# Kernel optimization log

Measured on AMD Instinct MI355X. Metric: run time of the kernel, lower is better.

The kernel has to match this reference:

```python
import jax, jax.numpy as jnp
import numpy as np

DECAY = 0.99
EPS = 1e-05
COMMIT = 0.25


def setup_inputs() -> dict:
    key = jax.random.key(0)
    k1, k2 = jax.random.split(key)
    dim, n_embed = 256, 8192
    z = jax.random.normal(k1, (32, 32, 32, dim), dtype=jnp.float32)
    embed = jax.random.normal(k2, (dim, n_embed), dtype=jnp.float32)
    cluster_size = jnp.zeros((n_embed,), dtype=jnp.float32)
    embed_avg = embed  # torch init: embed_avg = embed.clone()
    return {"z": z, "embed": embed, "cluster_size": cluster_size, "embed_avg": embed_avg}


def reference(z, embed, cluster_size, embed_avg):
    dim, n_embed = embed.shape
    flatten = z.reshape(-1, dim)                       # [N, D]
    # squared L2 distance to each code: ||f||^2 - 2 f.E + ||E||^2
    dist = ((flatten ** 2).sum(1, keepdims=True)
            - 2.0 * flatten @ embed
            + (embed ** 2).sum(0, keepdims=True))      # [N, K]
    ind = jnp.argmin(dist, axis=1)                     # [N]
    quantize = jnp.take(embed.T, ind, axis=0).reshape(z.shape)
    embed_ind = ind.reshape(z.shape[:-1])

    # EMA codebook update (training mode), via segment_sum instead of a dense one-hot
    counts = jax.ops.segment_sum(jnp.ones_like(ind, dtype=flatten.dtype), ind,
                                 num_segments=n_embed)          # [K]
    embed_sum = jax.ops.segment_sum(flatten, ind,
                                    num_segments=n_embed).T     # [D, K]
    cluster_size_new = cluster_size * DECAY + (1.0 - DECAY) * counts
    embed_avg_new = embed_avg * DECAY + (1.0 - DECAY) * embed_sum
    n = cluster_size_new.sum()
    cs = (cluster_size_new + EPS) / (n + n_embed * EPS) * n
    embed_new = embed_avg_new / cs[None, :]

    diff = COMMIT * jnp.mean((jax.lax.stop_gradient(quantize) - z) ** 2)
    quantize_st = z + jax.lax.stop_gradient(quantize - z)  # straight-through
    return quantize_st, diff, embed_ind, embed_new
```

## Files before the change

kernel.cpp:

```cpp
#include <hip/hip_runtime.h>
#include <hip/hip_bf16.h>

#define D 256
#define K 8192
#define NTOT 32768
#define BM 128
#define BN2 128
#define BD 32
#define CSPLIT 4
#define CT_PER (K / CSPLIT / BN2)

typedef __bf16 bf16x8 __attribute__((ext_vector_type(8)));
typedef float f32x4 __attribute__((ext_vector_type(4)));

__device__ __forceinline__ void gl_lds16(const void* g, void* l) {
    __builtin_amdgcn_global_load_lds(
        (__attribute__((address_space(1))) void*)(g),
        (__attribute__((address_space(3))) void*)(l), 16, 0, 0);
}

__device__ __forceinline__ unsigned int enc_f32(float f) {
    unsigned int u = __float_as_uint(f);
    return (u & 0x80000000u) ? ~u : (u | 0x80000000u);
}

__device__ __forceinline__ unsigned short f2bfu(float x) {
    __hip_bfloat16 h = __float2bfloat16(x);
    return __builtin_bit_cast(unsigned short, h);
}
__device__ __forceinline__ float bfu2f(unsigned short u) {
    return __bfloat162float(__builtin_bit_cast(__hip_bfloat16, u));
}

__global__ __launch_bounds__(256)
void conv_F(const float* __restrict__ z, unsigned short* __restrict__ Fhi,
            unsigned short* __restrict__ Flo) {
    int i4 = blockIdx.x * 256 + threadIdx.x;
    float4 v = ((const float4*)z)[i4];
    ushort4 h, l;
    h.x = f2bfu(v.x); l.x = f2bfu(v.x - bfu2f(h.x));
    h.y = f2bfu(v.y); l.y = f2bfu(v.y - bfu2f(h.y));
    h.z = f2bfu(v.z); l.z = f2bfu(v.z - bfu2f(h.z));
    h.w = f2bfu(v.w); l.w = f2bfu(v.w - bfu2f(h.w));
    ((ushort4*)Fhi)[i4] = h;
    ((ushort4*)Flo)[i4] = l;
}

__global__ __launch_bounds__(256)
void conv_E(const float* __restrict__ E, unsigned short* __restrict__ EhiT,
            unsigned short* __restrict__ EloT, float* __restrict__ ET,
            float* __restrict__ enorm) {
    __shared__ float tile[64][65];
    int tid = threadIdx.x;
    int k0 = blockIdx.x * 64, d0 = blockIdx.y * 64;
#pragma unroll
    for (int it = 0; it < 16; ++it) {
        int idx = it * 256 + tid;
        int dr = idx >> 6, kc = idx & 63;
        tile[kc][dr] = E[(d0 + dr) * K + k0 + kc];
    }
    __syncthreads();
#pragma unroll
    for (int it = 0; it < 16; ++it) {
        int idx = it * 256 + tid;
        int kr = idx >> 6, dc = idx & 63;
        float v = tile[kr][dc];
        unsigned short h = f2bfu(v);
        int o = (k0 + kr) * D + d0 + dc;
        EhiT[o] = h;
        EloT[o] = f2bfu(v - bfu2f(h));
        ET[o] = v;
        float p = v * v;
#pragma unroll
        for (int off = 32; off; off >>= 1) p += __shfl_down(p, off);
        if ((tid & 63) == 0) atomicAdd(&enorm[k0 + kr], p);
    }
}

__global__ __launch_bounds__(256)
void mfma_dist_argmin(const unsigned short* __restrict__ Fhi,
                      const unsigned short* __restrict__ Flo,
                      const unsigned short* __restrict__ EhiT,
                      const unsigned short* __restrict__ EloT,
                      const float* __restrict__ enorm,
                      unsigned long long* __restrict__ bestpack) {
    __shared__ unsigned short Ah[BM * BD], Al[BM * BD], Bh[BN2 * BD], Bl[BN2 * BD];

    const int tid = threadIdx.x;
    const int wave = tid >> 6;
    const int lane = tid & 63;
    const int qd = lane >> 4;
    const int ln = lane & 15;
    const int wm = (wave >> 1) * 64;
    const int wn = (wave & 1) * 64;
    const int n0 = blockIdx.x * BM;
    const int c0 = blockIdx.y * (K / CSPLIT);
    const int r_ = tid >> 2;
    const int s_sw = (tid & 3) ^ ((tid >> 3) & 3);
    const int csw = (qd ^ ((ln >> 1) & 3)) * 8;

    int aro[4], bro[4];
#pragma unroll
    for (int mi = 0; mi < 4; ++mi) aro[mi] = (wm + mi * 16 + ln) * BD + csw;
#pragma unroll
    for (int ni = 0; ni < 4; ++ni) bro[ni] = (wn + ni * 16 + ln) * BD + csw;

    float bestv[16];
    int besti[16];
#pragma unroll
    for (int i = 0; i < 16; ++i) { bestv[i] = 3.402823466e38f; besti[i] = 0; }

    for (int ct = 0; ct < CT_PER; ++ct) {
        const int cb = c0 + ct * BN2;
        f32x4 acc[4][4];
#pragma unroll
        for (int mi = 0; mi < 4; ++mi)
#pragma unroll
            for (int ni = 0; ni < 4; ++ni) acc[mi][ni] = (f32x4){0.f, 0.f, 0.f, 0.f};

        for (int d0 = 0; d0 < D; d0 += BD) {
            __syncthreads();
#pragma unroll
            for (int it = 0; it < 2; ++it) {
                const int ga = (n0 + it * 64 + r_) * D + d0 + s_sw * 8;
                const int gb = (cb + it * 64 + r_) * D + d0 + s_sw * 8;
                const int lo = it * 2048 + wave * 512;
                gl_lds16(Fhi + ga, &Ah[lo]);
                gl_lds16(Flo + ga, &Al[lo]);
                gl_lds16(EhiT + gb, &Bh[lo]);
                gl_lds16(EloT + gb, &Bl[lo]);
            }
            __syncthreads();

            bf16x8 a0[4], b0[4], b1[4];
#pragma unroll
            for (int mi = 0; mi < 4; ++mi) a0[mi] = *(const bf16x8*)&Ah[aro[mi]];
#pragma unroll
            for (int ni = 0; ni < 4; ++ni) b0[ni] = *(const bf16x8*)&Bh[bro[ni]];
#pragma unroll
            for (int mi = 0; mi < 4; ++mi)
#pragma unroll
                for (int ni = 0; ni < 4; ++ni)
                    acc[mi][ni] = __builtin_amdgcn_mfma_f32_16x16x32_bf16(
                        a0[mi], b0[ni], acc[mi][ni], 0, 0, 0);
#pragma unroll
            for (int ni = 0; ni < 4; ++ni) b1[ni] = *(const bf16x8*)&Bl[bro[ni]];
#pragma unroll
            for (int mi = 0; mi < 4; ++mi)
#pragma unroll
                for (int ni = 0; ni < 4; ++ni)
                    acc[mi][ni] = __builtin_amdgcn_mfma_f32_16x16x32_bf16(
                        a0[mi], b1[ni], acc[mi][ni], 0, 0, 0);
#pragma unroll
            for (int mi = 0; mi < 4; ++mi) a0[mi] = *(const bf16x8*)&Al[aro[mi]];
#pragma unroll
            for (int mi = 0; mi < 4; ++mi)
#pragma unroll
                for (int ni = 0; ni < 4; ++ni)
                    acc[mi][ni] = __builtin_amdgcn_mfma_f32_16x16x32_bf16(
                        a0[mi], b0[ni], acc[mi][ni], 0, 0, 0);
        }

#pragma unroll
        for (int ni = 0; ni < 4; ++ni) {
            int k = cb + wn + ni * 16 + ln;
            float en = enorm[k];
#pragma unroll
            for (int mi = 0; mi < 4; ++mi) {
                f32x4 a = acc[mi][ni];
#pragma unroll
                for (int r = 0; r < 4; ++r) {
                    float dist = en - 2.0f * a[r];
                    int bi = mi * 4 + r;
                    if (dist < bestv[bi]) { bestv[bi] = dist; besti[bi] = k; }
                }
            }
        }
    }

#pragma unroll
    for (int mi = 0; mi < 4; ++mi) {
#pragma unroll
        for (int r = 0; r < 4; ++r) {
            int bi = mi * 4 + r;
            float v = bestv[bi];
            int ix = besti[bi];
#pragma unroll
            for (int off = 1; off < 16; off <<= 1) {
                float v2 = __shfl_xor(v, off);
                int i2 = __shfl_xor(ix, off);
                if (v2 < v || (v2 == v && i2 < ix)) { v = v2; ix = i2; }
            }
            if (ln == 0) {
                int m = n0 + wm + mi * 16 + qd * 4 + r;
                unsigned long long pack =
                    ((unsigned long long)enc_f32(v) << 32) | (unsigned int)ix;
                atomicMin(&bestpack[m], pack);
            }
        }
    }
}

#define ROWS_PER_BLOCK 16
__global__ __launch_bounds__(256)
void assign_apply(const float* __restrict__ z,
                  const float* __restrict__ ET,
                  const unsigned long long* __restrict__ bestpack,
                  float* __restrict__ out_q, float* __restrict__ out_ind,
                  float* __restrict__ out_diff,
                  float* __restrict__ counts, float* __restrict__ esumT) {
    const int tx = threadIdx.x;
    const int rbase = blockIdx.x * ROWS_PER_BLOCK;
    float part = 0.f;
#pragma unroll 4
    for (int r = 0; r < ROWS_PER_BLOCK; ++r) {
        int n = rbase + r;
        unsigned long long p = bestpack[n];
        int idx = (int)(p & 0xFFFFFFFFull);
        float f = z[n * D + tx];
        float q = ET[idx * D + tx];
        out_q[n * D + tx] = q;
        float dd = q - f;
        part += dd * dd;
        atomicAdd(&esumT[idx * D + tx], f);
        if (tx == 0) {
            atomicAdd(&counts[idx], 1.0f);
            out_ind[n] = (float)idx;
        }
    }
#pragma unroll
    for (int off = 32; off; off >>= 1) part += __shfl_down(part, off);
    __shared__ float wsum[4];
    if ((tx & 63) == 0) wsum[tx >> 6] = part;
    __syncthreads();
    if (tx == 0) {
        float t = wsum[0] + wsum[1] + wsum[2] + wsum[3];
        atomicAdd(out_diff, t * (0.25f / 8388608.0f));
    }
}

__global__ __launch_bounds__(1024)
void csn_sum(const float* __restrict__ cs_in, const float* __restrict__ counts,
             float* __restrict__ csn, float* __restrict__ nsum) {
    const float decay = 0.99f;
    const float omd = 0.01f;
    int k = blockIdx.x * 1024 + threadIdx.x;
    float v = decay * cs_in[k] + omd * counts[k];
    csn[k] = v;
    float p = v;
#pragma unroll
    for (int off = 32; off; off >>= 1) p += __shfl_down(p, off);
    __shared__ float red[16];
    if ((threadIdx.x & 63) == 0) red[threadIdx.x >> 6] = p;
    __syncthreads();
    if (threadIdx.x == 0) {
        float t = 0.f;
#pragma unroll
        for (int i = 0; i < 16; ++i) t += red[i];
        atomicAdd(nsum, t);
    }
}

__global__ __launch_bounds__(256)
void finalize(const float* __restrict__ eavg, const float* __restrict__ esumT,
              const float* __restrict__ csn, const float* __restrict__ nsum,
              float* __restrict__ out_enew) {
    const float decay = 0.99f;
    const float omd = 0.01f;
    const float keps = (float)(8192 * 1e-5);
    int idx = blockIdx.x * 256 + threadIdx.x;
    float nv = nsum[0];
    int k = idx & (K - 1);
    int d = idx >> 13;
    float avg_new = decay * eavg[idx] + omd * esumT[k * D + d];
    float cs = (csn[k] + 1e-5f) / (nv + keps) * nv;
    out_enew[idx] = avg_new / cs;
}

extern "C" void kernel_launch(void* const* d_in, const int* in_sizes, int n_in,
                              void* d_out, int out_size, void* d_ws, size_t ws_size,
                              hipStream_t stream) {
    const float* z = (const float*)d_in[0];
    const float* embed = (const float*)d_in[1];
    const float* cs_in = (const float*)d_in[2];
    const float* eavg = (const float*)d_in[3];

    float* out = (float*)d_out;
    float* out_q = out;
    float* out_diff = out + 8388608;
    float* out_ind = out + 8388609;
    float* out_enew = out + 8421377;

    char* ws = (char*)d_ws;
    unsigned long long* bestpack = (unsigned long long*)ws;
    float* enorm = (float*)(ws + 262144);
    float* counts = (float*)(ws + 294912);
    float* csn = (float*)(ws + 327680);
    float* nsum = (float*)(ws + 360448);
    float* esumT = (float*)(ws + 360704);
    unsigned short* Fhi = (unsigned short*)(ws + 8749312);
    unsigned short* Flo = (unsigned short*)(ws + 25526528);
    unsigned short* EhiT = (unsigned short*)(ws + 42303744);
    unsigned short* EloT = (unsigned short*)(ws + 46498048);
    float* ET = (float*)(ws + 50692352);

    hipMemsetAsync(bestpack, 0xFF, NTOT * 8, stream);
    hipMemsetAsync(ws + 262144, 0, 8749312 - 262144, stream);
    hipMemsetAsync(out_diff, 0, 4, stream);

    conv_F<<<NTOT * D / 4 / 256, 256, 0, stream>>>(z, Fhi, Flo);
    conv_E<<<dim3(K / 64, D / 64), 256, 0, stream>>>(embed, EhiT, EloT, ET, enorm);
    mfma_dist_argmin<<<dim3(NTOT / BM, CSPLIT), 256, 0, stream>>>(Fhi, Flo, EhiT, EloT,
                                                                  enorm, bestpack);
    assign_apply<<<NTOT / ROWS_PER_BLOCK, 256, 0, stream>>>(z, ET, bestpack, out_q,
                                                            out_ind, out_diff, counts, esumT);
    csn_sum<<<K / 1024, 1024, 0, stream>>>(cs_in, counts, csn, nsum);
    finalize<<<(D * K) / 256, 256, 0, stream>>>(eavg, esumT, csn, nsum, out_enew);
}
```

Baseline: 600.0 us.

## Fuse conversion kernels, halve codebook split, vectorize assign and finalize, merge memsets

Merges the z and codebook bf16 split conversions into one launch, and halves the codebook split of the distance/argmin kernel so there are fewer blocks but each does more work. It hoists the code-norm loads ahead of the MFMA loop. The argmin packing switches to an inverted key with atomicMax so the workspace can be cleared with a single zero memset. The assign and finalize kernels are vectorized to float4 per lane, cutting launch and memory overhead at the cost of changed occupancy and access patterns.

After: 781.7 us. 30.3% more time.

```diff
diff --git a/kernel.cpp b/kernel.cpp
--- a/kernel.cpp
+++ b/kernel.cpp
@@ -7,7 +7,7 @@
 #define BM 128
 #define BN2 128
 #define BD 32
-#define CSPLIT 4
+#define CSPLIT 2
 #define CT_PER (K / CSPLIT / BN2)
 
 typedef __bf16 bf16x8 __attribute__((ext_vector_type(8)));
@@ -32,27 +32,29 @@
     return __bfloat162float(__builtin_bit_cast(__hip_bfloat16, u));
 }
 
+#define CONVF_BLOCKS (NTOT * D / 4 / 256)
 __global__ __launch_bounds__(256)
-void conv_F(const float* __restrict__ z, unsigned short* __restrict__ Fhi,
-            unsigned short* __restrict__ Flo) {
-    int i4 = blockIdx.x * 256 + threadIdx.x;
-    float4 v = ((const float4*)z)[i4];
-    ushort4 h, l;
-    h.x = f2bfu(v.x); l.x = f2bfu(v.x - bfu2f(h.x));
-    h.y = f2bfu(v.y); l.y = f2bfu(v.y - bfu2f(h.y));
-    h.z = f2bfu(v.z); l.z = f2bfu(v.z - bfu2f(h.z));
-    h.w = f2bfu(v.w); l.w = f2bfu(v.w - bfu2f(h.w));
-    ((ushort4*)Fhi)[i4] = h;
-    ((ushort4*)Flo)[i4] = l;
-}
-
-__global__ __launch_bounds__(256)
-void conv_E(const float* __restrict__ E, unsigned short* __restrict__ EhiT,
-            unsigned short* __restrict__ EloT, float* __restrict__ ET,
-            float* __restrict__ enorm) {
+void conv_all(const float* __restrict__ z, unsigned short* __restrict__ Fhi,
+              unsigned short* __restrict__ Flo, const float* __restrict__ E,
+              unsigned short* __restrict__ EhiT, unsigned short* __restrict__ EloT,
+              float* __restrict__ ET, float* __restrict__ enorm) {
+    int bx = blockIdx.x;
+    int tid = threadIdx.x;
+    if (bx < CONVF_BLOCKS) {
+        int i4 = bx * 256 + tid;
+        float4 v = ((const float4*)z)[i4];
+        ushort4 h, l;
+        h.x = f2bfu(v.x); l.x = f2bfu(v.x - bfu2f(h.x));
+        h.y = f2bfu(v.y); l.y = f2bfu(v.y - bfu2f(h.y));
+        h.z = f2bfu(v.z); l.z = f2bfu(v.z - bfu2f(h.z));
+        h.w = f2bfu(v.w); l.w = f2bfu(v.w - bfu2f(h.w));
+        ((ushort4*)Fhi)[i4] = h;
+        ((ushort4*)Flo)[i4] = l;
+        return;
+    }
     __shared__ float tile[64][65];
-    int tid = threadIdx.x;
-    int k0 = blockIdx.x * 64, d0 = blockIdx.y * 64;
+    int idx2 = bx - CONVF_BLOCKS;
+    int k0 = (idx2 & 127) * 64, d0 = (idx2 >> 7) * 64;
 #pragma unroll
     for (int it = 0; it < 16; ++it) {
         int idx = it * 256 + tid;
@@ -112,6 +114,10 @@
 
     for (int ct = 0; ct < CT_PER; ++ct) {
         const int cb = c0 + ct * BN2;
+        float en[4];
+#pragma unroll
+        for (int ni = 0; ni < 4; ++ni) en[ni] = enorm[cb + wn + ni * 16 + ln];
+
         f32x4 acc[4][4];
 #pragma unroll
         for (int mi = 0; mi < 4; ++mi)
@@ -164,13 +170,12 @@
 #pragma unroll
         for (int ni = 0; ni < 4; ++ni) {
             int k = cb + wn + ni * 16 + ln;
-            float en = enorm[k];
 #pragma unroll
             for (int mi = 0; mi < 4; ++mi) {
                 f32x4 a = acc[mi][ni];
 #pragma unroll
                 for (int r = 0; r < 4; ++r) {
-                    float dist = en - 2.0f * a[r];
+                    float dist = en[ni] - 2.0f * a[r];
                     int bi = mi * 4 + r;
                     if (dist < bestv[bi]) { bestv[bi] = dist; besti[bi] = k; }
                 }
@@ -193,15 +198,15 @@
             }
             if (ln == 0) {
                 int m = n0 + wm + mi * 16 + qd * 4 + r;
-                unsigned long long pack =
-                    ((unsigned long long)enc_f32(v) << 32) | (unsigned int)ix;
-                atomicMin(&bestpack[m], pack);
+                unsigned long long key =
+                    ((unsigned long long)(~enc_f32(v)) << 32) | (unsigned)(8191 - ix);
+                atomicMax(&bestpack[m], key);
             }
         }
     }
 }
 
-#define ROWS_PER_BLOCK 16
+#define AA_ROWS 32
 __global__ __launch_bounds__(256)
 void assign_apply(const float* __restrict__ z,
                   const float* __restrict__ ET,
@@ -209,21 +214,26 @@
                   float* __restrict__ out_q, float* __restrict__ out_ind,
                   float* __restrict__ out_diff,
                   float* __restrict__ counts, float* __restrict__ esumT) {
-    const int tx = threadIdx.x;
-    const int rbase = blockIdx.x * ROWS_PER_BLOCK;
+    const int wave = threadIdx.x >> 6;
+    const int lane = threadIdx.x & 63;
+    const int rbase = blockIdx.x * AA_ROWS + wave * (AA_ROWS / 4);
     float part = 0.f;
-#pragma unroll 4
-    for (int r = 0; r < ROWS_PER_BLOCK; ++r) {
+#pragma unroll
+    for (int r = 0; r < AA_ROWS / 4; ++r) {
         int n = rbase + r;
         unsigned long long p = bestpack[n];
-        int idx = (int)(p & 0xFFFFFFFFull);
-        float f = z[n * D + tx];
-        float q = ET[idx * D + tx];
-        out_q[n * D + tx] = q;
-        float dd = q - f;
-        part += dd * dd;
-        atomicAdd(&esumT[idx * D + tx], f);
-        if (tx == 0) {
+        int idx = 8191 - (int)(p & 0xFFFFFFFFull);
+        float4 f = ((const float4*)z)[n * 64 + lane];
+        float4 q = ((const float4*)ET)[idx * 64 + lane];
+        ((float4*)out_q)[n * 64 + lane] = q;
+        float dx = q.x - f.x, dy = q.y - f.y, dz = q.z - f.z, dw = q.w - f.w;
+        part += dx * dx + dy * dy + dz * dz + dw * dw;
+        float* eb = esumT + idx * D + lane * 4;
+        atomicAdd(eb + 0, f.x);
+        atomicAdd(eb + 1, f.y);
+        atomicAdd(eb + 2, f.z);
+        atomicAdd(eb + 3, f.w);
+        if (lane == 0) {
             atomicAdd(&counts[idx], 1.0f);
             out_ind[n] = (float)idx;
         }
@@ -231,9 +241,9 @@
 #pragma unroll
     for (int off = 32; off; off >>= 1) part += __shfl_down(part, off);
     __shared__ float wsum[4];
-    if ((tx & 63) == 0) wsum[tx >> 6] = part;
+    if (lane == 0) wsum[wave] = part;
     __syncthreads();
-    if (tx == 0) {
+    if (threadIdx.x == 0) {
         float t = wsum[0] + wsum[1] + wsum[2] + wsum[3];
         atomicAdd(out_diff, t * (0.25f / 8388608.0f));
     }
@@ -268,13 +278,22 @@
     const float decay = 0.99f;
     const float omd = 0.01f;
     const float keps = (float)(8192 * 1e-5);
-    int idx = blockIdx.x * 256 + threadIdx.x;
+    int i4 = blockIdx.x * 256 + threadIdx.x;
+    int e = i4 * 4;
+    int d = e >> 13;
+    int kb = e & (K - 1);
     float nv = nsum[0];
-    int k = idx & (K - 1);
-    int d = idx >> 13;
-    float avg_new = decay * eavg[idx] + omd * esumT[k * D + d];
-    float cs = (csn[k] + 1e-5f) / (nv + keps) * nv;
-    out_enew[idx] = avg_new / cs;
+    float4 ea = ((const float4*)eavg)[i4];
+    float4 cs4 = ((const float4*)csn)[kb >> 2];
+    float es0 = esumT[(kb + 0) * D + d];
+    float es1 = esumT[(kb + 1) * D + d];
+    float es2 = esumT[(kb + 2) * D + d];
+    float es3 = esumT[(kb + 3) * D + d];
+    float inv = 1.0f / (nv + keps);
+    out_enew[e + 0] = (decay * ea.x + omd * es0) / ((cs4.x + 1e-5f) * inv * nv);
+    out_enew[e + 1] = (decay * ea.y + omd * es1) / ((cs4.y + 1e-5f) * inv * nv);
+    out_enew[e + 2] = (decay * ea.z + omd * es2) / ((cs4.z + 1e-5f) * inv * nv);
+    out_enew[e + 3] = (decay * ea.w + omd * es3) / ((cs4.w + 1e-5f) * inv * nv);
 }
 
 extern "C" void kernel_launch(void* const* d_in, const int* in_sizes, int n_in,
@@ -304,16 +323,15 @@
     unsigned short* EloT = (unsigned short*)(ws + 46498048);
     float* ET = (float*)(ws + 50692352);
 
-    hipMemsetAsync(bestpack, 0xFF, NTOT * 8, stream);
-    hipMemsetAsync(ws + 262144, 0, 8749312 - 262144, stream);
+    hipMemsetAsync(ws, 0, 8749312, stream);
     hipMemsetAsync(out_diff, 0, 4, stream);
 
-    conv_F<<<NTOT * D / 4 / 256, 256, 0, stream>>>(z, Fhi, Flo);
-    conv_E<<<dim3(K / 64, D / 64), 256, 0, stream>>>(embed, EhiT, EloT, ET, enorm);
+    conv_all<<<CONVF_BLOCKS + 512, 256, 0, stream>>>(z, Fhi, Flo, embed, EhiT, EloT,
+                                                     ET, enorm);
     mfma_dist_argmin<<<dim3(NTOT / BM, CSPLIT), 256, 0, stream>>>(Fhi, Flo, EhiT, EloT,
                                                                   enorm, bestpack);
-    assign_apply<<<NTOT / ROWS_PER_BLOCK, 256, 0, stream>>>(z, ET, bestpack, out_q,
-                                                            out_ind, out_diff, counts, esumT);
+    assign_apply<<<NTOT / AA_ROWS, 256, 0, stream>>>(z, ET, bestpack, out_q,
+                                                     out_ind, out_diff, counts, esumT);
     csn_sum<<<K / 1024, 1024, 0, stream>>>(cs_in, counts, csn, nsum);
-    finalize<<<(D * K) / 256, 256, 0, stream>>>(eavg, esumT, csn, nsum, out_enew);
-}
+    finalize<<<(D * K / 4) / 256, 256, 0, stream>>>(eavg, esumT, csn, nsum, out_enew);
+}
```
